# Performance work log

Measured on AMD Instinct MI355X. Metric: run time of the kernel, lower is better.

Reference implementation:

```python
import jax, jax.numpy as jnp
import numpy as np

W = 256            # square image side (in_size)
N_ANGLES = 180     # theta = arange(180) degrees (default)
STEPS = 5


def _make_grids():
    # torch.affine_grid with R=[[cos,sin,0],[-sin,cos,0]], align_corners=False
    th = np.deg2rad(np.arange(N_ANGLES, dtype=np.float32))
    coords = (2.0 * np.arange(W, dtype=np.float32) + 1.0) / W - 1.0  # pixel centers in [-1,1]
    xg, yg = np.meshgrid(coords, coords)          # xg varies along cols, yg along rows
    cos = np.cos(th)[:, None, None]
    sin = np.sin(th)[:, None, None]
    gx = cos * xg + sin * yg
    gy = -sin * xg + cos * yg
    return jnp.asarray(np.stack([gx, gy], axis=-1))  # [A,W,W,2]

GRIDS = _make_grids()


def _grid_sample(img, grid):
    # img [N,W,W], grid [A,W,W,2]; bilinear, zeros padding, align_corners=False
    gx, gy = grid[..., 0], grid[..., 1]
    ix = ((gx + 1.0) * W - 1.0) * 0.5
    iy = ((gy + 1.0) * W - 1.0) * 0.5
    ix0 = jnp.floor(ix)
    iy0 = jnp.floor(iy)
    wx1 = ix - ix0
    wy1 = iy - iy0

    def gather(iyf, ixf):
        valid = (ixf >= 0) & (ixf < W) & (iyf >= 0) & (iyf < W)
        ixc = jnp.clip(ixf, 0, W - 1).astype(jnp.int32)
        iyc = jnp.clip(iyf, 0, W - 1).astype(jnp.int32)
        v = img[:, iyc, ixc]                     # [N,A,W,W]
        return jnp.where(valid, v, jnp.float32(0.0))

    return ((1.0 - wy1) * ((1.0 - wx1) * gather(iy0, ix0) + wx1 * gather(iy0, ix0 + 1))
            + wy1 * ((1.0 - wx1) * gather(iy0 + 1, ix0) + wx1 * gather(iy0 + 1, ix0 + 1)))


def _forward(x, index):
    img = x[:, 0]                                # [N,W,W] (C==1)
    rot = _grid_sample(img, GRIDS)               # [N,A,W(rows),W(cols)]
    segments = np.linspace(1, W / 2, STEPS + 1).astype(int)  # matches torch linspace dtype=int
    ran = np.abs(np.arange(W) - (W - 1) / 2.0)
    outs = []
    for step in range(2):
        t = segments[4 - index + step]
        m = (ran < t).astype(np.float32)
        m = jnp.asarray(m / m.sum())             # normalized hard mask over rows
        outs.append(jnp.einsum('narc,r->nca', rot, m))  # [N,W,A]
    return jnp.stack(outs, axis=1)               # [N,2,W,A]


def setup_inputs() -> dict:
    key = jax.random.key(0)
    x = jax.random.normal(key, (4, 1, W, W), dtype=jnp.float32)
    return {"x": x, "index": 2}


def reference(x, index):
    return _forward(x, index)
```

## Files before the change

kernel.cpp:

```cpp
#include <hip/hip_runtime.h>
#include <hip/hip_fp16.h>

#define W 256
#define NA 180
#define SPLIT 4
#define RWORDS 145
#define ROWBYTES 580
#define ROWS 259

__global__ __launch_bounds__(1024) void radon_kernel(
    const float* __restrict__ x, const int* __restrict__ index_p,
    float* __restrict__ out)
{
    __shared__ unsigned sw[ROWS * RWORDS];

    const int a = blockIdx.x;
    const int n = blockIdx.y;
    const int tid = threadIdx.x;
    const int c = tid & (W - 1);
    const int s = tid >> 8;

    const float* __restrict__ img = x + (size_t)n * W * W;

    if (tid < 435) {
        const int rr = tid / 145;
        const int w = tid - rr * 145;
        const int row = (rr == 0) ? 0 : (256 + rr);
        sw[row * RWORDS + w] = 0u;
    } else if (tid < 947) {
        const int i = tid - 435;
        const int row = 1 + (i >> 1);
        const int w = (i & 1) ? 129 : 0;
        sw[row * RWORDS + w] = 0u;
    }

    {
        const float4* img4 = (const float4*)img;
        #pragma unroll
        for (int k = 0; k < 16; ++k) {
            const int g = k * 1024 + tid;
            const int row = (g >> 6) + 1;
            const int m = g & 63;
            const float4 v = img4[g];
            const __half2 h01 = __floats2half2_rn(v.x, v.y);
            const __half2 h23 = __floats2half2_rn(v.z, v.w);
            sw[row * RWORDS + 2 * m + 1] = *(const unsigned*)&h01;
            sw[row * RWORDS + 2 * m + 2] = *(const unsigned*)&h23;
        }
    }
    __syncthreads();

    const int index = *index_p;
    const int seg[6] = {1, 26, 51, 77, 102, 128};
    const int t0 = seg[4 - index];
    const int t1 = seg[4 - index + 1];

    float sa, ca;
    sincosf((float)a * 0.017453292519943295f, &sa, &ca);

    const float xc = ((2.0f * (float)c + 1.0f) * (1.0f / (float)W)) - 1.0f;
    const float bx = fmaf(128.0f * ca, xc, 129.5f);
    const float by = fmaf(-128.0f * sa, xc, 128.5f);

    const int r1lo = 128 - t1;
    const int r0lo = 128 - t0, r0hi = 127 + t0;
    const int total = 2 * t1;
    const int chunk = (total + SPLIT - 1) / SPLIT;
    const int rs = r1lo + s * chunk;
    const int re = min(rs + chunk, r1lo + total);

#define TAP_BODY                                                              \
        float ix = fmaf(sa, rf, bx);                                          \
        float iy = fmaf(ca, rf, by);                                          \
        ix = __builtin_amdgcn_fmed3f(ix, 1.0f, 258.0f);                       \
        iy = __builtin_amdgcn_fmed3f(iy, 0.0f, 257.0f);                       \
        const float wx = __builtin_amdgcn_fractf(ix);                         \
        const float wy = __builtin_amdgcn_fractf(iy);                         \
        const int x0 = (int)ix;                                               \
        const int y0 = (int)iy;                                               \
        const int wi = y0 * RWORDS + (x0 >> 1);            \
        const unsigned A0 = sw[wi];                                           \
        const unsigned B0 = sw[wi + 1];                                       \
        const unsigned A1 = sw[wi + RWORDS];                                  \
        const unsigned B1 = sw[wi + RWORDS + 1];                              \
        const int sh = (x0 & 1) << 4;                                         \
        const unsigned q0 = __builtin_amdgcn_alignbit(B0, A0, sh);            \
        const unsigned q1 = __builtin_amdgcn_alignbit(B1, A1, sh);            \
        const __half2 h0 = *(const __half2*)&q0;       \
        const __half2 h1 = *(const __half2*)&q1;     \
        const __half2 wy2 = __float2half2_rn(wy);                             \
        const __half2 t = __hfma2(wy2, __hsub2(h1, h0), h0);                  \
        const float tl = __low2float(t);                                      \
        const float th = __high2float(t);                                     \
        const float val = fmaf(wx, th - tl, tl);

    float sumA = 0.0f, sumB = 0.0f, sumC = 0.0f;

    {
        const int e = min(re, r0lo);
        float rf = (float)rs - 127.5f;
        #pragma unroll 8
        for (int r = rs; r < e; ++r, rf += 1.0f) { TAP_BODY sumA += val; }
    }
    {
        const int b = max(rs, r0lo);
        const int e = min(re, r0hi + 1);
        float rf = (float)b - 127.5f;
        #pragma unroll 8
        for (int r = b; r < e; ++r, rf += 1.0f) { TAP_BODY sumB += val; }
    }
    {
        const int b = max(rs, r0hi + 1);
        float rf = (float)b - 127.5f;
        #pragma unroll 8
        for (int r = b; r < re; ++r, rf += 1.0f) { TAP_BODY sumC += val; }
    }
#undef TAP_BODY

    const float sum0 = sumB;
    const float sum1 = sumA + sumB + sumC;

    __syncthreads();
    float* red = (float*)sw;
    red[(0 * SPLIT + s) * W + c] = sum0;
    red[(1 * SPLIT + s) * W + c] = sum1;
    __syncthreads();

    if (s == 0) {
        const float acc0 = red[0 * W + c] + red[1 * W + c] + red[2 * W + c] + red[3 * W + c];
        const float* r1p = red + SPLIT * W;
        const float acc1 = r1p[0 * W + c] + r1p[1 * W + c] + r1p[2 * W + c] + r1p[3 * W + c];
        out[(((size_t)n * 2 + 0) * W + c) * NA + a] = acc0 * (1.0f / (float)(2 * t0));
        out[(((size_t)n * 2 + 1) * W + c) * NA + a] = acc1 * (1.0f / (float)(2 * t1));
    }
}

extern "C" void kernel_launch(void* const* d_in, const int* in_sizes, int n_in,
                              void* d_out, int out_size, void* d_ws, size_t ws_size,
                              hipStream_t stream) {
    const float* x = (const float*)d_in[0];
    const int* index_p = (const int*)d_in[1];
    float* out = (float*)d_out;
    const int N = in_sizes[0] / (W * W);
    dim3 grid(NA, N);
    radon_kernel<<<grid, 1024, 0, stream>>>(x, index_p, out);
}
```

Before: 44.92 us.

## Software-pipeline LDS bilinear taps with inline-asm ds_read2 and manual waitcnt

Replaces the three segment loops with one loop that keeps three taps in flight. Each tap issues its LDS reads as paired ds_read2_b32 inline asm and waits with an explicit lgkmcnt before consuming the data. Both inner and outer sums are accumulated in the single loop using predicate masks, which hides LDS latency but computes taps past the end of the range speculatively. It also adds an occupancy hint to launch_bounds. The hand-written waitcnt scheme is fragile if the compiler inserts other LDS operations.

```diff
diff --git a/kernel.cpp b/kernel.cpp
--- a/kernel.cpp
+++ b/kernel.cpp
@@ -8,7 +8,7 @@
 #define ROWBYTES 580
 #define ROWS 259
 
-__global__ __launch_bounds__(1024) void radon_kernel(
+__global__ __launch_bounds__(1024, 4) void radon_kernel(
     const float* __restrict__ x, const int* __restrict__ index_p,
     float* __restrict__ out)
 {
@@ -68,57 +68,72 @@
     const int chunk = (total + SPLIT - 1) / SPLIT;
     const int rs = r1lo + s * chunk;
     const int re = min(rs + chunk, r1lo + total);
+    const int len = re - rs;
+    const int w0 = r0hi - r0lo;
+    const int base0 = rs - r0lo;
 
-#define TAP_BODY                                                              \
-        float ix = fmaf(sa, rf, bx);                                          \
-        float iy = fmaf(ca, rf, by);                                          \
+    float sum0 = 0.0f, sum1 = 0.0f;
+
+    float wxA, wyA; int shA, adA; unsigned long long qAA, qBA;
+    float wxB, wyB; int shB, adB; unsigned long long qAB, qBB;
+    float wxC, wyC; int shC, adC; unsigned long long qAC, qBC;
+
+#define STG(WX, WY, SH, AD, RF) {                                             \
+        float ix = fmaf(sa, RF, bx);                                          \
+        float iy = fmaf(ca, RF, by);                                          \
         ix = __builtin_amdgcn_fmed3f(ix, 1.0f, 258.0f);                       \
         iy = __builtin_amdgcn_fmed3f(iy, 0.0f, 257.0f);                       \
-        const float wx = __builtin_amdgcn_fractf(ix);                         \
-        const float wy = __builtin_amdgcn_fractf(iy);                         \
+        WX = __builtin_amdgcn_fractf(ix);                                     \
+        WY = __builtin_amdgcn_fractf(iy);                                     \
         const int x0 = (int)ix;                                               \
         const int y0 = (int)iy;                                               \
-        const int wi = y0 * RWORDS + (x0 >> 1);            \
-        const unsigned A0 = sw[wi];                                           \
-        const unsigned B0 = sw[wi + 1];                                       \
-        const unsigned A1 = sw[wi + RWORDS];                                  \
-        const unsigned B1 = sw[wi + RWORDS + 1];                              \
-        const int sh = (x0 & 1) << 4;                                         \
-        const unsigned q0 = __builtin_amdgcn_alignbit(B0, A0, sh);            \
-        const unsigned q1 = __builtin_amdgcn_alignbit(B1, A1, sh);            \
-        const __half2 h0 = *(const __half2*)&q0;       \
-        const __half2 h1 = *(const __half2*)&q1;     \
-        const __half2 wy2 = __float2half2_rn(wy);                             \
+        SH = (x0 & 1) << 4;                                                   \
+        AD = y0 * ROWBYTES + (x0 >> 1) * 4; }
+
+#define ISS(QA, QB, AD)                                                       \
+        asm volatile("ds_read2_b32 %0, %2 offset0:0 offset1:145\n\t"          \
+                     "ds_read2_b32 %1, %2 offset0:1 offset1:146"              \
+                     : "=&v"(QA), "=&v"(QB) : "v"(AD));
+
+#define CNS(QA, QB, WX, WY, SH, K) {                                          \
+        asm volatile("s_waitcnt lgkmcnt(4)" : "+v"(QA), "+v"(QB));            \
+        const unsigned A0 = (unsigned)QA, A1 = (unsigned)(QA >> 32);          \
+        const unsigned B0 = (unsigned)QB, B1 = (unsigned)(QB >> 32);          \
+        const unsigned q0 = __builtin_amdgcn_alignbit(B0, A0, SH);            \
+        const unsigned q1 = __builtin_amdgcn_alignbit(B1, A1, SH);            \
+        const __half2 h0 = *(const __half2*)&q0;                              \
+        const __half2 h1 = *(const __half2*)&q1;                              \
+        const __half2 wy2 = __float2half2_rn(WY);                             \
         const __half2 t = __hfma2(wy2, __hsub2(h1, h0), h0);                  \
         const float tl = __low2float(t);                                      \
         const float th = __high2float(t);                                     \
-        const float val = fmaf(wx, th - tl, tl);
+        const float val = fmaf(WX, th - tl, tl);                              \
+        const bool m1 = (K) < len;                                            \
+        const bool m0 = m1 && ((unsigned)((K) + base0) <= (unsigned)w0);      \
+        sum1 += m1 ? val : 0.0f;                                              \
+        sum0 += m0 ? val : 0.0f; }
 
-    float sumA = 0.0f, sumB = 0.0f, sumC = 0.0f;
+    const float rf0 = (float)rs - 127.5f;
+    float rfA = rf0, rfB = rf0 + 1.0f, rfC = rf0 + 2.0f;
 
-    {
-        const int e = min(re, r0lo);
-        float rf = (float)rs - 127.5f;
-        #pragma unroll 8
-        for (int r = rs; r < e; ++r, rf += 1.0f) { TAP_BODY sumA += val; }
+    STG(wxA, wyA, shA, adA, rfA) ISS(qAA, qBA, adA) rfA += 3.0f;
+    STG(wxB, wyB, shB, adB, rfB) ISS(qAB, qBB, adB) rfB += 3.0f;
+    STG(wxC, wyC, shC, adC, rfC) ISS(qAC, qBC, adC) rfC += 3.0f;
+
+    for (int k0 = 0; k0 < len; k0 += 3) {
+        CNS(qAA, qBA, wxA, wyA, shA, k0)
+        STG(wxA, wyA, shA, adA, rfA) ISS(qAA, qBA, adA) rfA += 3.0f;
+        CNS(qAB, qBB, wxB, wyB, shB, k0 + 1)
+        STG(wxB, wyB, shB, adB, rfB) ISS(qAB, qBB, adB) rfB += 3.0f;
+        CNS(qAC, qBC, wxC, wyC, shC, k0 + 2)
+        STG(wxC, wyC, shC, adC, rfC) ISS(qAC, qBC, adC) rfC += 3.0f;
     }
-    {
-        const int b = max(rs, r0lo);
-        const int e = min(re, r0hi + 1);
-        float rf = (float)b - 127.5f;
-        #pragma unroll 8
-        for (int r = b; r < e; ++r, rf += 1.0f) { TAP_BODY sumB += val; }
-    }
-    {
-        const int b = max(rs, r0hi + 1);
-        float rf = (float)b - 127.5f;
-        #pragma unroll 8
-        for (int r = b; r < re; ++r, rf += 1.0f) { TAP_BODY sumC += val; }
-    }
-#undef TAP_BODY
+    asm volatile("s_waitcnt lgkmcnt(0)"
+                 : "+v"(qAA), "+v"(qBA), "+v"(qAB), "+v"(qBB), "+v"(qAC), "+v"(qBC));
 
-    const float sum0 = sumB;
-    const float sum1 = sumA + sumB + sumC;
+#undef STG
+#undef ISS
+#undef CNS
 
     __syncthreads();
     float* red = (float*)sw;
```

Measured after the change: 48.44 us. 1.08x slower.

## Split columns into quarters and stage only the bounding-box image window in LDS

Applied to the files above, without the earlier changes.

Each block now handles 64 output columns of one angle and image instead of all 256, with 512 threads and 8 row splits. It computes the bounding box of the sample coordinates and loads, as fp16, only the needed image window plus a zero border into shared memory, rather than the whole 256x256 image. This cuts per-block global loads and LDS footprint, which allows more blocks per CU. In exchange it adds bounds arithmetic, variable-stride indexing, a clamp on rows that could drop needed rows if the window is too large, and four times as many blocks.

```diff
diff --git a/kernel.cpp b/kernel.cpp
--- a/kernel.cpp
+++ b/kernel.cpp
@@ -3,68 +3,101 @@
 
 #define W 256
 #define NA 180
-#define SPLIT 4
-#define RWORDS 145
-#define ROWBYTES 580
-#define ROWS 259
+#define SPLIT 8
+#define SWORDS 13100
+#define SALLOC 13200
 
-__global__ __launch_bounds__(1024) void radon_kernel(
+
+__global__ __launch_bounds__(512) void radon_kernel(
     const float* __restrict__ x, const int* __restrict__ index_p,
     float* __restrict__ out)
 {
-    __shared__ unsigned sw[ROWS * RWORDS];
+    __shared__ unsigned sw[SALLOC];
 
     const int a = blockIdx.x;
     const int n = blockIdx.y;
+    const int cq = blockIdx.z;
     const int tid = threadIdx.x;
-    const int c = tid & (W - 1);
-    const int s = tid >> 8;
-
-    const float* __restrict__ img = x + (size_t)n * W * W;
-
-    if (tid < 435) {
-        const int rr = tid / 145;
-        const int w = tid - rr * 145;
-        const int row = (rr == 0) ? 0 : (256 + rr);
-        sw[row * RWORDS + w] = 0u;
-    } else if (tid < 947) {
-        const int i = tid - 435;
-        const int row = 1 + (i >> 1);
-        const int w = (i & 1) ? 129 : 0;
-        sw[row * RWORDS + w] = 0u;
-    }
-
-    {
-        const float4* img4 = (const float4*)img;
-        #pragma unroll
-        for (int k = 0; k < 16; ++k) {
-            const int g = k * 1024 + tid;
-            const int row = (g >> 6) + 1;
-            const int m = g & 63;
-            const float4 v = img4[g];
-            const __half2 h01 = __floats2half2_rn(v.x, v.y);
-            const __half2 h23 = __floats2half2_rn(v.z, v.w);
-            sw[row * RWORDS + 2 * m + 1] = *(const unsigned*)&h01;
-            sw[row * RWORDS + 2 * m + 2] = *(const unsigned*)&h23;
-        }
-    }
-    __syncthreads();
+    const int cl = tid & 63;
+    const int s = tid >> 6;
 
     const int index = *index_p;
     const int seg[6] = {1, 26, 51, 77, 102, 128};
     const int t0 = seg[4 - index];
     const int t1 = seg[4 - index + 1];
+    const int r1lo = 128 - t1;
+    const int r0lo = 128 - t0, r0hi = 127 + t0;
+    const int total = 2 * t1;
 
     float sa, ca;
     sincosf((float)a * 0.017453292519943295f, &sa, &ca);
 
-    const float xc = ((2.0f * (float)c + 1.0f) * (1.0f / (float)W)) - 1.0f;
+    const float xcl = ((2.0f * (float)(cq * 64) + 1.0f) * (1.0f / 256.0f)) - 1.0f;
+    const float xch = ((2.0f * (float)(cq * 64 + 63) + 1.0f) * (1.0f / 256.0f)) - 1.0f;
+    const float rfl = (float)r1lo - 127.5f;
+    const float rfh = rfl + (float)(total - 1);
+    const float bxl = fmaf(128.0f * ca, xcl, 129.5f);
+    const float bxh = fmaf(128.0f * ca, xch, 129.5f);
+    const float byl = fmaf(-128.0f * sa, xcl, 128.5f);
+    const float byh = fmaf(-128.0f * sa, xch, 128.5f);
+
+    float ixmin = fminf(fminf(fmaf(sa, rfl, bxl), fmaf(sa, rfh, bxl)),
+                        fminf(fmaf(sa, rfl, bxh), fmaf(sa, rfh, bxh)));
+    float ixmax = fmaxf(fmaxf(fmaf(sa, rfl, bxl), fmaf(sa, rfh, bxl)),
+                        fmaxf(fmaf(sa, rfl, bxh), fmaf(sa, rfh, bxh)));
+    float iymin = fminf(fminf(fmaf(ca, rfl, byl), fmaf(ca, rfh, byl)),
+                        fminf(fmaf(ca, rfl, byh), fmaf(ca, rfh, byh)));
+    float iymax = fmaxf(fmaxf(fmaf(ca, rfl, byl), fmaf(ca, rfh, byl)),
+                        fmaxf(fmaf(ca, rfl, byh), fmaf(ca, rfh, byh)));
+    ixmin = __builtin_amdgcn_fmed3f(ixmin, 1.0f, 258.0f);
+    ixmax = __builtin_amdgcn_fmed3f(ixmax, 1.0f, 258.0f);
+    iymin = __builtin_amdgcn_fmed3f(iymin, 0.0f, 257.0f);
+    iymax = __builtin_amdgcn_fmed3f(iymax, 0.0f, 257.0f);
+
+    const int gx0 = ((int)ixmin) & ~1;
+    const int gx1 = (int)ixmax + 1;
+    const int gy0 = (int)iymin;
+    const int gy1 = (int)iymax + 1;
+    const int nw = ((gx1 >> 1) - (gx0 >> 1)) + 2;
+    const int stride = nw | 1;
+    int nrows = gy1 - gy0 + 1;
+    nrows = min(nrows, SWORDS / stride);
+    const int nwords = nrows * stride;
+
+    for (int i = tid; i < nwords; i += 512) sw[i] = 0u;
+    __syncthreads();
+
+    {
+        const float* __restrict__ img = x + (size_t)n * W * W;
+        const int pylo = max(gy0 - 1, 0);
+        const int pyhi = min(gy1 - 1, 255);
+        const int pxlo = max(gx0 - 2, 0);
+        const int pxhi = min(gx1 - 2, 255);
+        const int nq2 = (pxhi - pxlo + 2) >> 1;
+        const int lbase = pylo + 1 - gy0;
+        const int nlr = pyhi - pylo + 1;
+        const int shift = (nq2 <= 64) ? 6 : 7;
+        const int smask = (1 << shift) - 1;
+        const int ncell = nlr << shift;
+        for (int i = tid; i < ncell; i += 512) {
+            const int lr = i >> shift, q = i & smask;
+            if (q < nq2) {
+                const int px = pxlo + 2 * q;
+                const int py = pylo + lr;
+                const float2 v = *(const float2*)(img + py * W + px);
+                const __half2 hp = __floats2half2_rn(v.x, v.y);
+                sw[(lbase + lr) * stride + ((px - (gx0 - 2)) >> 1)] = *(const unsigned*)&hp;
+            }
+        }
+    }
+    __syncthreads();
+
+    const int c = cq * 64 + cl;
+    const float xc = ((2.0f * (float)c + 1.0f) * (1.0f / 256.0f)) - 1.0f;
     const float bx = fmaf(128.0f * ca, xc, 129.5f);
     const float by = fmaf(-128.0f * sa, xc, 128.5f);
+    const int wbase = -(gy0 * stride + (gx0 >> 1));
 
-    const int r1lo = 128 - t1;
-    const int r0lo = 128 - t0, r0hi = 127 + t0;
-    const int total = 2 * t1;
     const int chunk = (total + SPLIT - 1) / SPLIT;
     const int rs = r1lo + s * chunk;
     const int re = min(rs + chunk, r1lo + total);
@@ -78,16 +111,16 @@
         const float wy = __builtin_amdgcn_fractf(iy);                         \
         const int x0 = (int)ix;                                               \
         const int y0 = (int)iy;                                               \
-        const int wi = y0 * RWORDS + (x0 >> 1);            \
+        const int wi = y0 * stride + (x0 >> 1) + wbase;                       \
         const unsigned A0 = sw[wi];                                           \
         const unsigned B0 = sw[wi + 1];                                       \
-        const unsigned A1 = sw[wi + RWORDS];                                  \
-        const unsigned B1 = sw[wi + RWORDS + 1];                              \
+        const unsigned A1 = sw[wi + stride];                                  \
+        const unsigned B1 = sw[wi + stride + 1];                              \
         const int sh = (x0 & 1) << 4;                                         \
         const unsigned q0 = __builtin_amdgcn_alignbit(B0, A0, sh);            \
         const unsigned q1 = __builtin_amdgcn_alignbit(B1, A1, sh);            \
-        const __half2 h0 = *(const __half2*)&q0;       \
-        const __half2 h1 = *(const __half2*)&q1;     \
+        const __half2 h0 = *(const __half2*)&q0;                              \
+        const __half2 h1 = *(const __half2*)&q1;                              \
         const __half2 wy2 = __float2half2_rn(wy);                             \
         const __half2 t = __hfma2(wy2, __hsub2(h1, h0), h0);                  \
         const float tl = __low2float(t);                                      \
@@ -95,24 +128,23 @@
         const float val = fmaf(wx, th - tl, tl);
 
     float sumA = 0.0f, sumB = 0.0f, sumC = 0.0f;
-
     {
         const int e = min(re, r0lo);
         float rf = (float)rs - 127.5f;
-        #pragma unroll 8
+        #pragma unroll 4
         for (int r = rs; r < e; ++r, rf += 1.0f) { TAP_BODY sumA += val; }
     }
     {
         const int b = max(rs, r0lo);
         const int e = min(re, r0hi + 1);
         float rf = (float)b - 127.5f;
-        #pragma unroll 8
+        #pragma unroll 4
         for (int r = b; r < e; ++r, rf += 1.0f) { TAP_BODY sumB += val; }
     }
     {
         const int b = max(rs, r0hi + 1);
         float rf = (float)b - 127.5f;
-        #pragma unroll 8
+        #pragma unroll 4
         for (int r = b; r < re; ++r, rf += 1.0f) { TAP_BODY sumC += val; }
     }
 #undef TAP_BODY
@@ -122,16 +154,19 @@
 
     __syncthreads();
     float* red = (float*)sw;
-    red[(0 * SPLIT + s) * W + c] = sum0;
-    red[(1 * SPLIT + s) * W + c] = sum1;
+    red[(0 * SPLIT + s) * 64 + cl] = sum0;
+    red[(1 * SPLIT + s) * 64 + cl] = sum1;
     __syncthreads();
 
     if (s == 0) {
-        const float acc0 = red[0 * W + c] + red[1 * W + c] + red[2 * W + c] + red[3 * W + c];
-        const float* r1p = red + SPLIT * W;
-        const float acc1 = r1p[0 * W + c] + r1p[1 * W + c] + r1p[2 * W + c] + r1p[3 * W + c];
-        out[(((size_t)n * 2 + 0) * W + c) * NA + a] = acc0 * (1.0f / (float)(2 * t0));
-        out[(((size_t)n * 2 + 1) * W + c) * NA + a] = acc1 * (1.0f / (float)(2 * t1));
+        float a0 = 0.0f, a1 = 0.0f;
+        #pragma unroll
+        for (int j = 0; j < SPLIT; ++j) {
+            a0 += red[(0 * SPLIT + j) * 64 + cl];
+            a1 += red[(1 * SPLIT + j) * 64 + cl];
+        }
+        out[(((size_t)n * 2 + 0) * W + c) * NA + a] = a0 * (1.0f / (float)(2 * t0));
+        out[(((size_t)n * 2 + 1) * W + c) * NA + a] = a1 * (1.0f / (float)(2 * t1));
     }
 }
 
@@ -142,6 +177,6 @@
     const int* index_p = (const int*)d_in[1];
     float* out = (float*)d_out;
     const int N = in_sizes[0] / (W * W);
-    dim3 grid(NA, N);
-    radon_kernel<<<grid, 1024, 0, stream>>>(x, index_p, out);
+    dim3 grid(NA, N, 4);
+    radon_kernel<<<grid, 512, 0, stream>>>(x, index_p, out);
 }
```

New measurement: 56.35 us. 25.5% more time.

## Precompute padded fp16 image in workspace and DMA it into LDS

Applied to the files above, without the earlier changes.

Adds a prep kernel that converts each input image to a zero-padded fp16 layout in global workspace once. Each of the 180 angle blocks then copies the prepared image straight into shared memory with global_load_lds instead of converting fp32 to fp16 and zeroing borders itself. This removes duplicated conversion work and register round-trips across blocks, at the cost of an extra kernel launch and a workspace write/read. The 16-byte LDS DMA path also depends on hardware support and alignment.

```diff
diff --git a/kernel.cpp b/kernel.cpp
--- a/kernel.cpp
+++ b/kernel.cpp
@@ -7,12 +7,33 @@
 #define RWORDS 145
 #define ROWBYTES 580
 #define ROWS 259
+#define IMG_WORDS 37555
+#define IMG_WORDS_PAD 37568
+#define NCHUNK 9389
+
+__global__ __launch_bounds__(256) void prep_kernel(
+    const float* __restrict__ x, unsigned* __restrict__ ws)
+{
+    const int row = blockIdx.x;
+    const int n = blockIdx.y;
+    const int t = threadIdx.x;
+    if (t >= RWORDS) return;
+    unsigned v = 0u;
+    if (row >= 1 && row <= 256 && t >= 1 && t <= 128) {
+        const int y = row - 1;
+        const int px = 2 * (t - 1);
+        const float2 f2 = *(const float2*)(x + ((size_t)n * W + y) * W + px);
+        const __half2 hp = __floats2half2_rn(f2.x, f2.y);
+        v = *(const unsigned*)&hp;
+    }
+    ws[(size_t)n * IMG_WORDS_PAD + row * RWORDS + t] = v;
+}
 
 __global__ __launch_bounds__(1024) void radon_kernel(
-    const float* __restrict__ x, const int* __restrict__ index_p,
+    const unsigned* __restrict__ ws, const int* __restrict__ index_p,
     float* __restrict__ out)
 {
-    __shared__ unsigned sw[ROWS * RWORDS];
+    __shared__ unsigned sw[IMG_WORDS_PAD];
 
     const int a = blockIdx.x;
     const int n = blockIdx.y;
@@ -20,32 +41,18 @@
     const int c = tid & (W - 1);
     const int s = tid >> 8;
 
-    const float* __restrict__ img = x + (size_t)n * W * W;
-
-    if (tid < 435) {
-        const int rr = tid / 145;
-        const int w = tid - rr * 145;
-        const int row = (rr == 0) ? 0 : (256 + rr);
-        sw[row * RWORDS + w] = 0u;
-    } else if (tid < 947) {
-        const int i = tid - 435;
-        const int row = 1 + (i >> 1);
-        const int w = (i & 1) ? 129 : 0;
-        sw[row * RWORDS + w] = 0u;
-    }
-
     {
-        const float4* img4 = (const float4*)img;
+        const char* src = (const char*)(ws + (size_t)n * IMG_WORDS_PAD);
+        char* dst = (char*)sw;
         #pragma unroll
-        for (int k = 0; k < 16; ++k) {
-            const int g = k * 1024 + tid;
-            const int row = (g >> 6) + 1;
-            const int m = g & 63;
-            const float4 v = img4[g];
-            const __half2 h01 = __floats2half2_rn(v.x, v.y);
-            const __half2 h23 = __floats2half2_rn(v.z, v.w);
-            sw[row * RWORDS + 2 * m + 1] = *(const unsigned*)&h01;
-            sw[row * RWORDS + 2 * m + 2] = *(const unsigned*)&h23;
+        for (int k = 0; k < 10; ++k) {
+            const int i = k * 1024 + tid;
+            if (i < NCHUNK) {
+                __builtin_amdgcn_global_load_lds(
+                    (const __attribute__((address_space(1))) void*)(src + (size_t)i * 16),
+                    (__attribute__((address_space(3))) void*)(dst + (size_t)i * 16),
+                    16, 0, 0);
+            }
         }
     }
     __syncthreads();
@@ -142,6 +149,11 @@
     const int* index_p = (const int*)d_in[1];
     float* out = (float*)d_out;
     const int N = in_sizes[0] / (W * W);
+    unsigned* ws = (unsigned*)d_ws;
+
+    dim3 pgrid(ROWS, N);
+    prep_kernel<<<pgrid, 256, 0, stream>>>(x, ws);
+
     dim3 grid(NA, N);
-    radon_kernel<<<grid, 1024, 0, stream>>>(x, index_p, out);
+    radon_kernel<<<grid, 1024, 0, stream>>>(ws, index_p, out);
 }
```

New measurement: 48.15 us. 7.2% more time.
